# Kernel tuning notes

Hardware: AMD Instinct MI355X
Metric: run time of the kernel (lower is better)

The kernel has to match this reference:

```python
import jax, jax.numpy as jnp
import numpy as np

MARGIN = 1.0
NUM_CLASSES = 64

def setup_inputs() -> dict:
    key = jax.random.key(0)
    k1, k2 = jax.random.split(key)
    embeddings = jax.random.normal(k1, (4096, 512), dtype=jnp.float32)
    labels = jax.random.randint(k2, (4096,), 0, NUM_CLASSES, dtype=jnp.int64)
    return {"embeddings": embeddings, "labels": labels}

def _pairwise_dist(x):
    # Euclidean cdist via GEMM: ||xi||^2 + ||xj||^2 - 2 xi.xj, with a
    # grad-safe sqrt (zero distance -> zero, no nan gradient).
    sq_norms = jnp.sum(x * x, axis=1)                      # [B]
    sq = sq_norms[:, None] + sq_norms[None, :] - 2.0 * (x @ x.T)
    sq = jnp.maximum(sq, 0.0)
    pos = sq > 0.0
    return jnp.where(pos, jnp.sqrt(jnp.where(pos, sq, 1.0)), 0.0)

def reference(embeddings, labels):
    B = embeddings.shape[0]
    # L2 normalize (normalize=True)
    emb = embeddings / jnp.maximum(
        jnp.linalg.norm(embeddings, axis=1, keepdims=True), 1e-12)
    dist = _pairwise_dist(emb)                             # [B, B]
    same = labels[:, None] == labels[None, :]              # [B, B]
    eye = jnp.eye(B, dtype=bool)
    pos_mask = same & ~eye
    neg_mask = ~same
    pos_cnt = jnp.sum(pos_mask, axis=1)                    # [B]
    neg_cnt = jnp.sum(neg_mask, axis=1)
    # hard_positive=False -> mean over positive distances
    pos_stat = jnp.sum(jnp.where(pos_mask, dist, 0.0), axis=1) / jnp.maximum(pos_cnt, 1)
    # hardest negative = masked min (infinity trick)
    neg_stat = jnp.min(jnp.where(neg_mask, dist, jnp.inf), axis=1)
    per_row = jnp.maximum(pos_stat - neg_stat + MARGIN, 0.0)
    valid = (pos_cnt > 0) & (neg_cnt > 0)
    n_valid = jnp.sum(valid)
    total = jnp.sum(jnp.where(valid, per_row, 0.0))
    # reduction='mean' over valid rows; 0.0 if none valid
    return jnp.where(n_valid > 0, total / jnp.maximum(n_valid, 1), 0.0)
```

## Files before the change

### kernel.cpp

```cpp
#include <hip/hip_runtime.h>
#include <hip/hip_bf16.h>

#define BSZ 4096
#define DIM 512
#define NCLS 64
#define MARGIN_F 1.0f
#define NT 32
#define NPAIR (NT * (NT + 1) / 2)
#define NBLK (NPAIR * 2)
#define NSL (2 * NT)
#define NFIN 16
#define BK 64
#define NKS (DIM / BK)

typedef float floatx4 __attribute__((ext_vector_type(4)));
typedef unsigned char u8;

#define OFF_PP  (BSZ * DIM)
#define OFF_PN  (OFF_PP + NSL * BSZ * 4)
#define OFF_ACC (OFF_PN + NSL * BSZ * 4)

__device__ __forceinline__ void gld_lds16(const u8* g, u8* l) {
    __builtin_amdgcn_global_load_lds(
        (const __attribute__((address_space(1))) unsigned int*)g,
        (__attribute__((address_space(3))) unsigned int*)l, 16, 0, 0);
}

__global__ __launch_bounds__(256) void ht_normalize(
        const float* __restrict__ emb, u8* __restrict__ ebf,
        float* __restrict__ acc_total, int* __restrict__ acc_nv,
        int* __restrict__ counter2) {
    const int lane = threadIdx.x & 63;
    const int row = blockIdx.x * 4 + (threadIdx.x >> 6);
    const float4* r4 = (const float4*)(emb + (size_t)row * DIM);
    float4 v0 = r4[lane * 2];
    float4 v1 = r4[lane * 2 + 1];
    float s = v0.x * v0.x + v0.y * v0.y + v0.z * v0.z + v0.w * v0.w
            + v1.x * v1.x + v1.y * v1.y + v1.z * v1.z + v1.w * v1.w;
#pragma unroll
    for (int off = 1; off < 64; off <<= 1) s += __shfl_xor(s, off);
    const float inv = 1.0f / fmaxf(sqrtf(s), 1e-12f);

    int d0 = 0, d1 = 0;
    d0 = __builtin_amdgcn_cvt_pk_fp8_f32(v0.x * inv, v0.y * inv, d0, 0);
    d0 = __builtin_amdgcn_cvt_pk_fp8_f32(v0.z * inv, v0.w * inv, d0, 1);
    d1 = __builtin_amdgcn_cvt_pk_fp8_f32(v1.x * inv, v1.y * inv, d1, 0);
    d1 = __builtin_amdgcn_cvt_pk_fp8_f32(v1.z * inv, v1.w * inv, d1, 1);
    uint2 o; o.x = (unsigned)d0; o.y = (unsigned)d1;
    ((uint2*)(ebf + (size_t)row * DIM))[lane] = o;

    if (blockIdx.x == 0 && threadIdx.x == 0) {
        *acc_total = 0.0f; *acc_nv = 0; *counter2 = 0;
    }
}

__global__ __launch_bounds__(256) void ht_gemm_reduce(
        const u8* __restrict__ ebf, const int* __restrict__ labels,
        float* __restrict__ part_ps, unsigned* __restrict__ part_nm) {
    __shared__ u8 sA[2][64 * BK];
    __shared__ u8 sB[2][128 * BK];
    __shared__ int sLI[64];
    __shared__ int sLJ[128];
    __shared__ float sCPps[128];
    __shared__ float sCPnm[128];

    const int p = blockIdx.x >> 1;
    const int h2 = blockIdx.x & 1;
    int rem = p, by = 0;
    while (rem >= NT - by) { rem -= NT - by; ++by; }
    const int bx = by + rem;
    const bool offd = (bx != by);

    const int t = threadIdx.x;
    const int row0 = by * 128 + h2 * 64;
    const int col0 = bx * 128;

    if (t < 64) sLI[t] = labels[row0 + t];
    else if (t < 192) sLJ[t - 64] = labels[col0 + (t - 64)];

    const int lane = t & 63;
    const int wave = t >> 6;
    const int wr = (wave >> 1) * 32;
    const int wc = (wave & 1) * 64;
    const int l15 = lane & 15;
    const int quad = lane >> 4;

    const int sa = t;
    const int ga = (sa & 3) ^ ((sa >> 3) & 3);
    const u8* gA0 = ebf + (size_t)(row0 + (sa >> 2)) * DIM + ga * 16;
    const int sb0 = t, sb1 = 256 + t;
    const int gb0 = (sb0 & 3) ^ ((sb0 >> 3) & 3);
    const int gb1 = (sb1 & 3) ^ ((sb1 >> 3) & 3);
    const u8* gB0 = ebf + (size_t)(col0 + (sb0 >> 2)) * DIM + gb0 * 16;
    const u8* gB1 = ebf + (size_t)(col0 + (sb1 >> 2)) * DIM + gb1 * 16;
    const int lbA = wave * 64 * 16;
    const int lbB0 = wave * 64 * 16;
    const int lbB1 = (256 + wave * 64) * 16;

    floatx4 acc[2][4] = {};

    gld_lds16(gA0, &sA[0][lbA]);
    gld_lds16(gB0, &sB[0][lbB0]);
    gld_lds16(gB1, &sB[0][lbB1]);

    int cur = 0;
    for (int ks = 0; ks < NKS; ++ks) {
        __syncthreads();
        if (ks + 1 < NKS) {
            const int kb = (ks + 1) * BK;
            gld_lds16(gA0 + kb, &sA[cur ^ 1][lbA]);
            gld_lds16(gB0 + kb, &sB[cur ^ 1][lbB0]);
            gld_lds16(gB1 + kb, &sB[cur ^ 1][lbB1]);
        }
#pragma unroll
        for (int h = 0; h < 2; ++h) {
            const int co = (((h * 2 + (quad >> 1)) ^ ((l15 >> 1) & 3)) * 16)
                         + (quad & 1) * 8;
            long af[2]; long bf[4];
#pragma unroll
            for (int mi = 0; mi < 2; ++mi)
                af[mi] = *(const long*)(&sA[cur][(wr + mi * 16 + l15) * BK + co]);
#pragma unroll
            for (int ni = 0; ni < 4; ++ni)
                bf[ni] = *(const long*)(&sB[cur][(wc + ni * 16 + l15) * BK + co]);
#pragma unroll
            for (int mi = 0; mi < 2; ++mi)
#pragma unroll
                for (int ni = 0; ni < 4; ++ni)
                    acc[mi][ni] = __builtin_amdgcn_mfma_f32_16x16x32_fp8_fp8(
                        af[mi], bf[ni], acc[mi][ni], 0, 0, 0);
        }
        cur ^= 1;
    }

    const float INF = __uint_as_float(0x7F800000u);
    const int rslice = 2 * bx + (wc >> 6);
    float psc[4] = {0.f, 0.f, 0.f, 0.f};
    float nmc[4] = {INF, INF, INF, INF};
#pragma unroll
    for (int mi = 0; mi < 2; ++mi) {
        const int rbase = wr + mi * 16 + quad * 4;
#pragma unroll
        for (int r = 0; r < 4; ++r) {
            const int rloc = rbase + r;
            const int gi = row0 + rloc;
            const int rl = sLI[rloc];
            float ps = 0.0f, nm = INF;
#pragma unroll
            for (int ni = 0; ni < 4; ++ni) {
                const int cloc = wc + ni * 16 + l15;
                const int gj = col0 + cloc;
                const int cl = sLJ[cloc];
                const float d = __builtin_amdgcn_sqrtf(
                    fmaxf(2.0f - 2.0f * acc[mi][ni][r], 0.0f));
                if (rl == cl) {
                    if (gi != gj) ps += d;
                    if (offd) psc[ni] += d;
                } else {
                    nm = fminf(nm, d);
                    if (offd) nmc[ni] = fminf(nmc[ni], d);
                }
            }
#pragma unroll
            for (int off = 1; off < 16; off <<= 1) {
                ps += __shfl_xor(ps, off);
                nm = fminf(nm, __shfl_xor(nm, off));
            }
            if (l15 == 0) {
                part_ps[rslice * BSZ + gi] = ps;
                part_nm[rslice * BSZ + gi] = __float_as_uint(nm);
            }
        }
    }
    if (offd) {
        const int cslice = 2 * by + h2;
        float cps[4], cnm[4];
#pragma unroll
        for (int ni = 0; ni < 4; ++ni) {
            float ps = psc[ni], nm = nmc[ni];
            ps += __shfl_xor(ps, 16); ps += __shfl_xor(ps, 32);
            nm = fminf(nm, __shfl_xor(nm, 16));
            nm = fminf(nm, __shfl_xor(nm, 32));
            cps[ni] = ps; cnm[ni] = nm;
        }
        if (wave >= 2 && quad == 0) {
#pragma unroll
            for (int ni = 0; ni < 4; ++ni) {
                const int cl = wc + ni * 16 + l15;
                sCPps[cl] = cps[ni];
                sCPnm[cl] = cnm[ni];
            }
        }
        __syncthreads();
        if (wave < 2 && quad == 0) {
#pragma unroll
            for (int ni = 0; ni < 4; ++ni) {
                const int cl = wc + ni * 16 + l15;
                const int gj = col0 + cl;
                const float ps = cps[ni] + sCPps[cl];
                const float nm = fminf(cnm[ni], sCPnm[cl]);
                part_ps[cslice * BSZ + gj] = ps;
                part_nm[cslice * BSZ + gj] = __float_as_uint(nm);
            }
        }
    }
}

__global__ __launch_bounds__(256) void ht_finalize(
        const float* __restrict__ part_ps, const unsigned* __restrict__ part_nm,
        const int* __restrict__ labels, float* __restrict__ acc_total,
        int* __restrict__ acc_nv, int* __restrict__ counter2,
        float* __restrict__ out) {
    __shared__ int hist[NCLS];
    __shared__ float sT[4];
    __shared__ int sN[4];
    const int t = threadIdx.x;
    if (t < NCLS) hist[t] = 0;
    __syncthreads();
    for (int i = t; i < BSZ; i += 256) atomicAdd(&hist[labels[i]], 1);
    __syncthreads();

    const int j = blockIdx.x * 256 + t;
    float ps = 0.0f;
    float nm = __uint_as_float(0x7F800000u);
#pragma unroll 8
    for (int s = 0; s < NSL; ++s) {
        ps += part_ps[s * BSZ + j];
        nm = fminf(nm, __uint_as_float(part_nm[s * BSZ + j]));
    }
    const int cnt = hist[labels[j]];
    const int pc = cnt - 1;
    const int nc = BSZ - cnt;
    float loss = 0.0f;
    int lv = 0;
    if (pc > 0 && nc > 0) {
        loss = fmaxf(ps / (float)pc - nm + MARGIN_F, 0.0f);
        lv = 1;
    }
#pragma unroll
    for (int off = 1; off < 64; off <<= 1) {
        loss += __shfl_xor(loss, off);
        lv += __shfl_xor(lv, off);
    }
    if ((t & 63) == 0) { sT[t >> 6] = loss; sN[t >> 6] = lv; }
    __syncthreads();
    if (t == 0) {
        const float tt = sT[0] + sT[1] + sT[2] + sT[3];
        const int nn = sN[0] + sN[1] + sN[2] + sN[3];
        __hip_atomic_fetch_add(acc_total, tt, __ATOMIC_ACQ_REL,
                               __HIP_MEMORY_SCOPE_AGENT);
        __hip_atomic_fetch_add(acc_nv, nn, __ATOMIC_ACQ_REL,
                               __HIP_MEMORY_SCOPE_AGENT);
        const int old2 = __hip_atomic_fetch_add(counter2, 1, __ATOMIC_ACQ_REL,
                                                __HIP_MEMORY_SCOPE_AGENT);
        if (old2 == NFIN - 1) {
            const float ft = __hip_atomic_load(acc_total, __ATOMIC_ACQUIRE,
                                               __HIP_MEMORY_SCOPE_AGENT);
            const int fn = __hip_atomic_load(acc_nv, __ATOMIC_ACQUIRE,
                                             __HIP_MEMORY_SCOPE_AGENT);
            out[0] = (fn > 0) ? ft / (float)fn : 0.0f;
        }
    }
}

extern "C" void kernel_launch(void* const* d_in, const int* in_sizes, int n_in,
                              void* d_out, int out_size, void* d_ws, size_t ws_size,
                              hipStream_t stream) {
    const float* emb = (const float*)d_in[0];
    const int* labels = (const int*)d_in[1];
    float* out = (float*)d_out;
    char* ws = (char*)d_ws;

    u8* ebf = (u8*)ws;
    float* part_ps = (float*)(ws + OFF_PP);
    unsigned* part_nm = (unsigned*)(ws + OFF_PN);
    float* acc_total = (float*)(ws + OFF_ACC);
    int* acc_nv = (int*)(ws + OFF_ACC + 4);
    int* counter2 = (int*)(ws + OFF_ACC + 8);

    ht_normalize<<<BSZ / 4, 256, 0, stream>>>(emb, ebf, acc_total, acc_nv,
                                              counter2);
    ht_gemm_reduce<<<NBLK, 256, 0, stream>>>(ebf, labels, part_ps, part_nm);
    ht_finalize<<<NFIN, 256, 0, stream>>>(part_ps, part_nm, labels,
                                          acc_total, acc_nv, counter2, out);
}
```

Baseline: 86.90 us.

## Fuse normalize, GEMM-reduce and finalize into one cooperative kernel with grid syncs

The three kernels (normalize, tiled FP8 GEMM with masked row reductions, and finalize) are merged into one cooperative launch of NBLK blocks, separated by grid-wide barriers. This targets the launch gaps and per-kernel ramp-up between stages. It sets launch bounds to 5 blocks per CU so the whole grid can be co-resident, which may cap registers for the GEMM body and risk spills. Grid syncs add their own cost. If the occupancy query shows the grid cannot be co-resident, the code falls back to the original three launches.

```diff
diff --git a/kernel.cpp b/kernel.cpp
--- a/kernel.cpp
+++ b/kernel.cpp
@@ -1,5 +1,8 @@
 #include <hip/hip_runtime.h>
 #include <hip/hip_bf16.h>
+#include <hip/hip_cooperative_groups.h>
+
+namespace cg = cooperative_groups;
 
 #define BSZ 4096
 #define DIM 512
@@ -26,12 +29,12 @@
         (__attribute__((address_space(3))) unsigned int*)l, 16, 0, 0);
 }
 
-__global__ __launch_bounds__(256) void ht_normalize(
-        const float* __restrict__ emb, u8* __restrict__ ebf,
-        float* __restrict__ acc_total, int* __restrict__ acc_nv,
-        int* __restrict__ counter2) {
-    const int lane = threadIdx.x & 63;
-    const int row = blockIdx.x * 4 + (threadIdx.x >> 6);
+__device__ __forceinline__ void normalize_body(
+        const float* __restrict__ emb, u8* __restrict__ ebf, int blk,
+        float* acc_total, int* acc_nv, int* counter2) {
+    const int t = threadIdx.x;
+    const int lane = t & 63;
+    const int row = blk * 4 + (t >> 6);
     const float4* r4 = (const float4*)(emb + (size_t)row * DIM);
     float4 v0 = r4[lane * 2];
     float4 v1 = r4[lane * 2 + 1];
@@ -49,23 +52,16 @@
     uint2 o; o.x = (unsigned)d0; o.y = (unsigned)d1;
     ((uint2*)(ebf + (size_t)row * DIM))[lane] = o;
 
-    if (blockIdx.x == 0 && threadIdx.x == 0) {
-        *acc_total = 0.0f; *acc_nv = 0; *counter2 = 0;
-    }
-}
-
-__global__ __launch_bounds__(256) void ht_gemm_reduce(
+    if (blk == 0 && t == 0) { *acc_total = 0.0f; *acc_nv = 0; *counter2 = 0; }
+}
+
+__device__ __forceinline__ void gemm_body(
         const u8* __restrict__ ebf, const int* __restrict__ labels,
-        float* __restrict__ part_ps, unsigned* __restrict__ part_nm) {
-    __shared__ u8 sA[2][64 * BK];
-    __shared__ u8 sB[2][128 * BK];
-    __shared__ int sLI[64];
-    __shared__ int sLJ[128];
-    __shared__ float sCPps[128];
-    __shared__ float sCPnm[128];
-
-    const int p = blockIdx.x >> 1;
-    const int h2 = blockIdx.x & 1;
+        float* __restrict__ part_ps, unsigned* __restrict__ part_nm, int blk,
+        u8 (*sA)[64 * BK], u8 (*sB)[128 * BK],
+        int* sLI, int* sLJ, float* sCPps, float* sCPnm) {
+    const int p = blk >> 1;
+    const int h2 = blk & 1;
     int rem = p, by = 0;
     while (rem >= NT - by) { rem -= NT - by; ++by; }
     const int bx = by + rem;
@@ -99,6 +95,7 @@
 
     floatx4 acc[2][4] = {};
 
+    __syncthreads();
     gld_lds16(gA0, &sA[0][lbA]);
     gld_lds16(gB0, &sB[0][lbB0]);
     gld_lds16(gB1, &sB[0][lbB1]);
@@ -206,21 +203,17 @@
     }
 }
 
-__global__ __launch_bounds__(256) void ht_finalize(
+__device__ __forceinline__ void finalize_body(
         const float* __restrict__ part_ps, const unsigned* __restrict__ part_nm,
-        const int* __restrict__ labels, float* __restrict__ acc_total,
-        int* __restrict__ acc_nv, int* __restrict__ counter2,
-        float* __restrict__ out) {
-    __shared__ int hist[NCLS];
-    __shared__ float sT[4];
-    __shared__ int sN[4];
+        const int* __restrict__ labels, float* acc_total, int* acc_nv,
+        int* counter2, float* out, int blk, int* hist, float* sT, int* sN) {
     const int t = threadIdx.x;
     if (t < NCLS) hist[t] = 0;
     __syncthreads();
     for (int i = t; i < BSZ; i += 256) atomicAdd(&hist[labels[i]], 1);
     __syncthreads();
 
-    const int j = blockIdx.x * 256 + t;
+    const int j = blk * 256 + t;
     float ps = 0.0f;
     float nm = __uint_as_float(0x7F800000u);
 #pragma unroll 8
@@ -263,6 +256,68 @@
     }
 }
 
+__global__ __launch_bounds__(256, 5) void ht_fused(
+        const float* __restrict__ emb, const int* __restrict__ labels,
+        u8* __restrict__ ebf,
+        float* __restrict__ part_ps, unsigned* __restrict__ part_nm,
+        float* __restrict__ acc_total, int* __restrict__ acc_nv,
+        int* __restrict__ counter2, float* __restrict__ out) {
+    __shared__ u8 sA[2][64 * BK];
+    __shared__ u8 sB[2][128 * BK];
+    __shared__ int sLI[128];
+    __shared__ int sLJ[128];
+    __shared__ float sCPps[128];
+    __shared__ float sCPnm[128];
+    __shared__ float sT[4];
+    __shared__ int sN[4];
+
+    if (blockIdx.x < BSZ / 4)
+        normalize_body(emb, ebf, blockIdx.x, acc_total, acc_nv, counter2);
+
+    cg::this_grid().sync();
+
+    gemm_body(ebf, labels, part_ps, part_nm, blockIdx.x,
+              sA, sB, sLI, sLJ, sCPps, sCPnm);
+
+    cg::this_grid().sync();
+
+    if (blockIdx.x < NFIN)
+        finalize_body(part_ps, part_nm, labels, acc_total, acc_nv, counter2,
+                      out, blockIdx.x, sLI, sT, sN);
+}
+
+__global__ __launch_bounds__(256) void ht_normalize(
+        const float* __restrict__ emb, u8* __restrict__ ebf,
+        float* __restrict__ acc_total, int* __restrict__ acc_nv,
+        int* __restrict__ counter2) {
+    normalize_body(emb, ebf, blockIdx.x, acc_total, acc_nv, counter2);
+}
+
+__global__ __launch_bounds__(256) void ht_gemm_reduce(
+        const u8* __restrict__ ebf, const int* __restrict__ labels,
+        float* __restrict__ part_ps, unsigned* __restrict__ part_nm) {
+    __shared__ u8 sA[2][64 * BK];
+    __shared__ u8 sB[2][128 * BK];
+    __shared__ int sLI[128];
+    __shared__ int sLJ[128];
+    __shared__ float sCPps[128];
+    __shared__ float sCPnm[128];
+    gemm_body(ebf, labels, part_ps, part_nm, blockIdx.x,
+              sA, sB, sLI, sLJ, sCPps, sCPnm);
+}
+
+__global__ __launch_bounds__(256) void ht_finalize(
+        const float* __restrict__ part_ps, const unsigned* __restrict__ part_nm,
+        const int* __restrict__ labels, float* __restrict__ acc_total,
+        int* __restrict__ acc_nv, int* __restrict__ counter2,
+        float* __restrict__ out) {
+    __shared__ int hist[NCLS];
+    __shared__ float sT[4];
+    __shared__ int sN[4];
+    finalize_body(part_ps, part_nm, labels, acc_total, acc_nv, counter2,
+                  out, blockIdx.x, hist, sT, sN);
+}
+
 extern "C" void kernel_launch(void* const* d_in, const int* in_sizes, int n_in,
                               void* d_out, int out_size, void* d_ws, size_t ws_size,
                               hipStream_t stream) {
@@ -278,9 +333,24 @@
     int* acc_nv = (int*)(ws + OFF_ACC + 4);
     int* counter2 = (int*)(ws + OFF_ACC + 8);
 
-    ht_normalize<<<BSZ / 4, 256, 0, stream>>>(emb, ebf, acc_total, acc_nv,
-                                              counter2);
-    ht_gemm_reduce<<<NBLK, 256, 0, stream>>>(ebf, labels, part_ps, part_nm);
-    ht_finalize<<<NFIN, 256, 0, stream>>>(part_ps, part_nm, labels,
-                                          acc_total, acc_nv, counter2, out);
-}
+    int maxb = 0;
+    hipError_t qerr = hipOccupancyMaxActiveBlocksPerMultiprocessor(
+        &maxb, (const void*)ht_fused, 256, 0);
+    const bool coop_ok = (qerr == hipSuccess) && (maxb * 256 >= NBLK);
+
+    if (coop_ok) {
+        void* args[] = {
+            (void*)&emb, (void*)&labels, (void*)&ebf,
+            (void*)&part_ps, (void*)&part_nm,
+            (void*)&acc_total, (void*)&acc_nv, (void*)&counter2, (void*)&out,
+        };
+        hipLaunchCooperativeKernel((const void*)ht_fused, dim3(NBLK), dim3(256),
+                                   args, 0, stream);
+    } else {
+        ht_normalize<<<BSZ / 4, 256, 0, stream>>>(emb, ebf, acc_total, acc_nv,
+                                                  counter2);
+        ht_gemm_reduce<<<NBLK, 256, 0, stream>>>(ebf, labels, part_ps, part_nm);
+        ht_finalize<<<NFIN, 256, 0, stream>>>(part_ps, part_nm, labels,
+                                              acc_total, acc_nv, counter2, out);
+    }
+}
```

New measurement: 87.15 us. About the same (+0.3%).

## Shrink GEMM tiles to 64x64 symmetric blocks and reduce row partials in LDS

Applied to the files above, without the earlier changes.

Switches the symmetric-tile FP8 GEMM from 64x128 half-tiles over 32 column tiles to 64x64 tiles over a 64x64 upper-triangular grid. This gives 2080 blocks with half the LDS each, and adds an occupancy hint of 8 blocks per CU. Row partials from the two column-waves are now combined in LDS before a single store, so there is one slice per tile column (64 slices). The intent is more parallelism, better occupancy and smaller per-block tail work, at the cost of less operand reuse per loaded byte and an extra barrier.

```diff
diff --git a/kernel.cpp b/kernel.cpp
--- a/kernel.cpp
+++ b/kernel.cpp
@@ -5,10 +5,9 @@
 #define DIM 512
 #define NCLS 64
 #define MARGIN_F 1.0f
-#define NT 32
-#define NPAIR (NT * (NT + 1) / 2)
-#define NBLK (NPAIR * 2)
-#define NSL (2 * NT)
+#define NT2 64
+#define NBLK (NT2 * (NT2 + 1) / 2)
+#define NSL 64
 #define NFIN 16
 #define BK 64
 #define NKS (DIM / BK)
@@ -54,79 +53,71 @@
     }
 }
 
-__global__ __launch_bounds__(256) void ht_gemm_reduce(
+__global__ __launch_bounds__(256, 8) void ht_gemm_reduce(
         const u8* __restrict__ ebf, const int* __restrict__ labels,
         float* __restrict__ part_ps, unsigned* __restrict__ part_nm) {
     __shared__ u8 sA[2][64 * BK];
-    __shared__ u8 sB[2][128 * BK];
+    __shared__ u8 sB[2][64 * BK];
     __shared__ int sLI[64];
-    __shared__ int sLJ[128];
-    __shared__ float sCPps[128];
-    __shared__ float sCPnm[128];
-
-    const int p = blockIdx.x >> 1;
-    const int h2 = blockIdx.x & 1;
-    int rem = p, by = 0;
-    while (rem >= NT - by) { rem -= NT - by; ++by; }
+    __shared__ int sLJ[64];
+    __shared__ float sRps[64];
+    __shared__ float sRnm[64];
+    __shared__ float sCps[64];
+    __shared__ float sCnm[64];
+
+    int rem = blockIdx.x, by = 0;
+    while (rem >= NT2 - by) { rem -= NT2 - by; ++by; }
     const int bx = by + rem;
     const bool offd = (bx != by);
 
     const int t = threadIdx.x;
-    const int row0 = by * 128 + h2 * 64;
-    const int col0 = bx * 128;
+    const int row0 = by * 64;
+    const int col0 = bx * 64;
 
     if (t < 64) sLI[t] = labels[row0 + t];
-    else if (t < 192) sLJ[t - 64] = labels[col0 + (t - 64)];
+    else if (t < 128) sLJ[t - 64] = labels[col0 + (t - 64)];
 
     const int lane = t & 63;
     const int wave = t >> 6;
     const int wr = (wave >> 1) * 32;
-    const int wc = (wave & 1) * 64;
+    const int wc = (wave & 1) * 32;
     const int l15 = lane & 15;
     const int quad = lane >> 4;
 
     const int sa = t;
     const int ga = (sa & 3) ^ ((sa >> 3) & 3);
     const u8* gA0 = ebf + (size_t)(row0 + (sa >> 2)) * DIM + ga * 16;
-    const int sb0 = t, sb1 = 256 + t;
-    const int gb0 = (sb0 & 3) ^ ((sb0 >> 3) & 3);
-    const int gb1 = (sb1 & 3) ^ ((sb1 >> 3) & 3);
-    const u8* gB0 = ebf + (size_t)(col0 + (sb0 >> 2)) * DIM + gb0 * 16;
-    const u8* gB1 = ebf + (size_t)(col0 + (sb1 >> 2)) * DIM + gb1 * 16;
-    const int lbA = wave * 64 * 16;
-    const int lbB0 = wave * 64 * 16;
-    const int lbB1 = (256 + wave * 64) * 16;
-
-    floatx4 acc[2][4] = {};
-
-    gld_lds16(gA0, &sA[0][lbA]);
-    gld_lds16(gB0, &sB[0][lbB0]);
-    gld_lds16(gB1, &sB[0][lbB1]);
+    const u8* gB0 = ebf + (size_t)(col0 + (sa >> 2)) * DIM + ga * 16;
+    const int lb = wave * 64 * 16;
+
+    floatx4 acc[2][2] = {};
+
+    gld_lds16(gA0, &sA[0][lb]);
+    gld_lds16(gB0, &sB[0][lb]);
 
     int cur = 0;
     for (int ks = 0; ks < NKS; ++ks) {
         __syncthreads();
         if (ks + 1 < NKS) {
             const int kb = (ks + 1) * BK;
-            gld_lds16(gA0 + kb, &sA[cur ^ 1][lbA]);
-            gld_lds16(gB0 + kb, &sB[cur ^ 1][lbB0]);
-            gld_lds16(gB1 + kb, &sB[cur ^ 1][lbB1]);
+            gld_lds16(gA0 + kb, &sA[cur ^ 1][lb]);
+            gld_lds16(gB0 + kb, &sB[cur ^ 1][lb]);
         }
 #pragma unroll
         for (int h = 0; h < 2; ++h) {
             const int co = (((h * 2 + (quad >> 1)) ^ ((l15 >> 1) & 3)) * 16)
                          + (quad & 1) * 8;
-            long af[2]; long bf[4];
+            long af[2]; long bf[2];
 #pragma unroll
             for (int mi = 0; mi < 2; ++mi)
                 af[mi] = *(const long*)(&sA[cur][(wr + mi * 16 + l15) * BK + co]);
 #pragma unroll
-            for (int ni = 0; ni < 4; ++ni)
+            for (int ni = 0; ni < 2; ++ni)
                 bf[ni] = *(const long*)(&sB[cur][(wc + ni * 16 + l15) * BK + co]);
 #pragma unroll
             for (int mi = 0; mi < 2; ++mi)
 #pragma unroll
-                for (int ni = 0; ni < 4; ++ni)
+                for (int ni = 0; ni < 2; ++ni)
                     acc[mi][ni] = __builtin_amdgcn_mfma_f32_16x16x32_fp8_fp8(
                         af[mi], bf[ni], acc[mi][ni], 0, 0, 0);
         }
@@ -134,20 +125,19 @@
     }
 
     const float INF = __uint_as_float(0x7F800000u);
-    const int rslice = 2 * bx + (wc >> 6);
-    float psc[4] = {0.f, 0.f, 0.f, 0.f};
-    float nmc[4] = {INF, INF, INF, INF};
+    float rowPS[2][4], rowNM[2][4];
+    float colPS[2] = {0.f, 0.f};
+    float colNM[2] = {INF, INF};
 #pragma unroll
     for (int mi = 0; mi < 2; ++mi) {
-        const int rbase = wr + mi * 16 + quad * 4;
 #pragma unroll
         for (int r = 0; r < 4; ++r) {
-            const int rloc = rbase + r;
+            const int rloc = wr + mi * 16 + quad * 4 + r;
             const int gi = row0 + rloc;
             const int rl = sLI[rloc];
             float ps = 0.0f, nm = INF;
 #pragma unroll
-            for (int ni = 0; ni < 4; ++ni) {
+            for (int ni = 0; ni < 2; ++ni) {
                 const int cloc = wc + ni * 16 + l15;
                 const int gj = col0 + cloc;
                 const int cl = sLJ[cloc];
@@ -155,10 +145,10 @@
                     fmaxf(2.0f - 2.0f * acc[mi][ni][r], 0.0f));
                 if (rl == cl) {
                     if (gi != gj) ps += d;
-                    if (offd) psc[ni] += d;
+                    if (offd) colPS[ni] += d;
                 } else {
                     nm = fminf(nm, d);
-                    if (offd) nmc[ni] = fminf(nmc[ni], d);
+                    if (offd) colNM[ni] = fminf(colNM[ni], d);
                 }
             }
 #pragma unroll
@@ -166,42 +156,59 @@
                 ps += __shfl_xor(ps, off);
                 nm = fminf(nm, __shfl_xor(nm, off));
             }
-            if (l15 == 0) {
-                part_ps[rslice * BSZ + gi] = ps;
-                part_nm[rslice * BSZ + gi] = __float_as_uint(nm);
-            }
-        }
+            rowPS[mi][r] = ps;
+            rowNM[mi][r] = nm;
+        }
+    }
+    if ((wave & 1) && l15 == 0) {
+#pragma unroll
+        for (int mi = 0; mi < 2; ++mi)
+#pragma unroll
+            for (int r = 0; r < 4; ++r) {
+                const int rloc = wr + mi * 16 + quad * 4 + r;
+                sRps[rloc] = rowPS[mi][r];
+                sRnm[rloc] = rowNM[mi][r];
+            }
+    }
+    __syncthreads();
+    if (!(wave & 1) && l15 == 0) {
+#pragma unroll
+        for (int mi = 0; mi < 2; ++mi)
+#pragma unroll
+            for (int r = 0; r < 4; ++r) {
+                const int rloc = wr + mi * 16 + quad * 4 + r;
+                const int gi = row0 + rloc;
+                part_ps[bx * BSZ + gi] = rowPS[mi][r] + sRps[rloc];
+                part_nm[bx * BSZ + gi] = __float_as_uint(
+                    fminf(rowNM[mi][r], sRnm[rloc]));
+            }
     }
     if (offd) {
-        const int cslice = 2 * by + h2;
-        float cps[4], cnm[4];
-#pragma unroll
-        for (int ni = 0; ni < 4; ++ni) {
-            float ps = psc[ni], nm = nmc[ni];
-            ps += __shfl_xor(ps, 16); ps += __shfl_xor(ps, 32);
-            nm = fminf(nm, __shfl_xor(nm, 16));
-            nm = fminf(nm, __shfl_xor(nm, 32));
-            cps[ni] = ps; cnm[ni] = nm;
+#pragma unroll
+        for (int ni = 0; ni < 2; ++ni) {
+            colPS[ni] += __shfl_xor(colPS[ni], 16);
+            colPS[ni] += __shfl_xor(colPS[ni], 32);
+            colNM[ni] = fminf(colNM[ni], __shfl_xor(colNM[ni], 16));
+            colNM[ni] = fminf(colNM[ni], __shfl_xor(colNM[ni], 32));
         }
         if (wave >= 2 && quad == 0) {
 #pragma unroll
-            for (int ni = 0; ni < 4; ++ni) {
-                const int cl = wc + ni * 16 + l15;
-                sCPps[cl] = cps[ni];
-                sCPnm[cl] = cnm[ni];
-            }
-        }
-        __syncthreads();
-        if (wave < 2 && quad == 0) {
-#pragma unroll
-            for (int ni = 0; ni < 4; ++ni) {
-                const int cl = wc + ni * 16 + l15;
-                const int gj = col0 + cl;
-                const float ps = cps[ni] + sCPps[cl];
-                const float nm = fminf(cnm[ni], sCPnm[cl]);
-                part_ps[cslice * BSZ + gj] = ps;
-                part_nm[cslice * BSZ + gj] = __float_as_uint(nm);
-            }
+            for (int ni = 0; ni < 2; ++ni) {
+                const int cloc = wc + ni * 16 + l15;
+                sCps[cloc] = colPS[ni];
+                sCnm[cloc] = colNM[ni];
+            }
+        }
+    }
+    __syncthreads();
+    if (offd && wave < 2 && quad == 0) {
+#pragma unroll
+        for (int ni = 0; ni < 2; ++ni) {
+            const int cloc = wc + ni * 16 + l15;
+            const int gj = col0 + cloc;
+            part_ps[by * BSZ + gj] = colPS[ni] + sCps[cloc];
+            part_nm[by * BSZ + gj] = __float_as_uint(
+                fminf(colNM[ni], sCnm[cloc]));
         }
     }
 }
```

New measurement: 89.88 us. 1.03x slower.
